# Performance work log

Hardware: AMD Instinct MI355X
Metric: run time of the kernel (lower is better)

Reference implementation:

```python
import jax, jax.numpy as jnp
import numpy as np

H = 8      # hidden_size
IN = 14    # input_size
B = 4096   # batch
T = 512    # seq_len
BN_EPS = 1e-5


def setup_inputs() -> dict:
    key = jax.random.key(0)
    ks = jax.random.split(key, 16)
    s = lambda k, shape, scale=0.25: jax.random.normal(k, shape, jnp.float32) * scale
    return {
        "x": jax.random.normal(ks[0], (B, T, IN), jnp.float32),
        # layer 1 LSTM params (PyTorch gate order: i, f, g, o)
        "Wih1": s(ks[1], (4 * H, IN)), "Whh1": s(ks[2], (4 * H, H)),
        "bih1": s(ks[3], (4 * H,)), "bhh1": s(ks[4], (4 * H,)),
        # layer 2 LSTM params
        "Wih2": s(ks[5], (4 * H, H)), "Whh2": s(ks[6], (4 * H, H)),
        "bih2": s(ks[7], (4 * H,)), "bhh2": s(ks[8], (4 * H,)),
        # BatchNorm1d(H) params + running stats (eval mode)
        "bn_gamma": jnp.ones((H,), jnp.float32), "bn_beta": jnp.zeros((H,), jnp.float32),
        "bn_mean": s(ks[9], (H,), 0.01), "bn_var": jnp.ones((H,), jnp.float32),
        # MLP head
        "w1": s(ks[10], (4, H)), "b1": s(ks[11], (4,)),
        "w2": s(ks[12], (1, 4)), "b2": s(ks[13], (1,)),
    }


def _cell(gates, c):
    # gates: [B, 4H] pre-activation, PyTorch order i, f, g, o
    i, f, g, o = jnp.split(gates, 4, axis=-1)
    c_new = jax.nn.sigmoid(f) * c + jax.nn.sigmoid(i) * jnp.tanh(g)
    h_new = jax.nn.sigmoid(o) * jnp.tanh(c_new)
    return h_new, c_new


def _lstm_last(x, Wih1, Whh1, bih1, bhh1, Wih2, Whh2, bih2, bhh2):
    # x: [B, T, IN] -> returns last hidden state of layer 2: [B, H]
    xt = jnp.swapaxes(x, 0, 1)  # [T, B, IN]
    # precompute input projections for layer 1 in one big GEMM
    xp1 = jnp.einsum('tbf,gf->tbg', xt, Wih1) + (bih1 + bhh1)  # [T, B, 4H]
    b2sum = bih2 + bhh2
    Bn = x.shape[0]
    z = jnp.zeros((Bn, H), x.dtype)
    init = (z, z, z, z)  # h1, c1, h2, c2

    def step(carry, xp):
        h1, c1, h2, c2 = carry
        h1, c1 = _cell(xp + h1 @ Whh1.T, c1)
        h2, c2 = _cell(h1 @ Wih2.T + h2 @ Whh2.T + b2sum, c2)
        return (h1, c1, h2, c2), None

    (h1, c1, h2, c2), _ = jax.lax.scan(step, init, xp1)
    return h2


def reference(x, Wih1, Whh1, bih1, bhh1, Wih2, Whh2, bih2, bhh2,
              bn_gamma, bn_beta, bn_mean, bn_var, w1, b1, w2, b2):
    last = _lstm_last(x, Wih1, Whh1, bih1, bhh1, Wih2, Whh2, bih2, bhh2)  # [B, H]
    # BatchNorm1d in eval mode (running stats); dropout is identity in eval
    normed = bn_gamma * (last - bn_mean) / jnp.sqrt(bn_var + BN_EPS) + bn_beta
    h = jax.nn.relu(normed @ w1.T + b1)  # [B, 4]
    out = h @ w2.T + b2                  # [B, 1]
    return out.squeeze(-1)               # [B]
```

## Files before the change

### kernel.cpp

```cpp
#include <hip/hip_runtime.h>

#define T_SEQ 512
#define INPUT 14
#define HID 8
#define GATES 32
#define TC 16
#define NCHUNK (T_SEQ / TC)
#define BN_EPS 1e-5f

__device__ __forceinline__ float fast_exp2(float x) { return __builtin_amdgcn_exp2f(x); }
__device__ __forceinline__ float fast_rcp(float x)  { return __builtin_amdgcn_rcpf(x); }

__global__ __launch_bounds__(256, 2)
void lstm_forex_kernel(const float* __restrict__ x,
                       const float* __restrict__ Wih1, const float* __restrict__ Whh1,
                       const float* __restrict__ bih1, const float* __restrict__ bhh1,
                       const float* __restrict__ Wih2, const float* __restrict__ Whh2,
                       const float* __restrict__ bih2, const float* __restrict__ bhh2,
                       const float* __restrict__ bn_gamma, const float* __restrict__ bn_beta,
                       const float* __restrict__ bn_mean, const float* __restrict__ bn_var,
                       const float* __restrict__ w1p, const float* __restrict__ b1p,
                       const float* __restrict__ w2p, const float* __restrict__ b2p,
                       float* __restrict__ out)
{
    __shared__ float xbuf[4][2][TC][16];
    __shared__ float gbuf[4][2][GATES];
    __shared__ float hbuf1[4][2][8];
    __shared__ float hbuf2[4][2][8];

    const int tid  = threadIdx.x;
    const int wave = tid >> 6;
    const int lane = tid & 63;
    const int grp  = lane >> 5;
    const int g    = lane & 31;
    const int unit = g & 7;
    const int type = g >> 3;

    const int b = blockIdx.x * 8 + wave * 2 + grp;

    float wi1[INPUT], wh1[HID], wi2[HID], wh2[HID];
#pragma unroll
    for (int k = 0; k < INPUT; ++k) wi1[k] = Wih1[g * INPUT + k];
#pragma unroll
    for (int j = 0; j < HID; ++j) wh1[j] = Whh1[g * HID + j];
#pragma unroll
    for (int j = 0; j < HID; ++j) wi2[j] = Wih2[g * HID + j];
#pragma unroll
    for (int j = 0; j < HID; ++j) wh2[j] = Whh2[g * HID + j];
    const float bsum1 = bih1[g] + bhh1[g];
    const float bsum2 = bih2[g] + bhh2[g];

    const float actScale = (type == 2) ? -2.885390082f : -1.4426950408f;
    const float actMul   = (type == 2) ? 2.f : 1.f;
    const float actAdd   = (type == 2) ? -1.f : 0.f;

    const float* gptr[7];
    int loff[7];
#pragma unroll
    for (int it = 0; it < 7; ++it) {
        int d   = it * 64 + lane;
        int es  = d / 224;
        int idx = d - es * 224;
        int tr  = idx / 14;
        int k   = idx - tr * 14;
        int bb  = blockIdx.x * 8 + wave * 2 + es;
        gptr[it] = x + (size_t)bb * (T_SEQ * INPUT) + idx;
        loff[it] = es * (TC * 16) + tr * 16 + k;
    }

    float h1[HID], h2v[HID];
    float c1 = 0.f, c2 = 0.f;
#pragma unroll
    for (int j = 0; j < HID; ++j) { h1[j] = 0.f; h2v[j] = 0.f; }

    float st[7];
#pragma unroll
    for (int it = 0; it < 7; ++it) { st[it] = *gptr[it]; gptr[it] += TC * INPUT; }

    float (*xw)[TC][16] = xbuf[wave];
    float* gw  = gbuf[wave][grp];
    float* h1w = hbuf1[wave][grp];
    float* h2w = hbuf2[wave][grp];

    for (int c = 0; c < NCHUNK; ++c) {
#pragma unroll
        for (int it = 0; it < 7; ++it) ((float*)xw)[loff[it]] = st[it];
        if (c + 1 < NCHUNK) {
#pragma unroll
            for (int it = 0; it < 7; ++it) { st[it] = *gptr[it]; gptr[it] += TC * INPUT; }
        }
        __builtin_amdgcn_wave_barrier();

#pragma unroll
        for (int t = 0; t < TC; ++t) {
            const float* xrow = &xw[grp][t][0];
            float4 xa = *(const float4*)(xrow + 0);
            float4 xb = *(const float4*)(xrow + 4);
            float4 xc = *(const float4*)(xrow + 8);
            float2 xd = *(const float2*)(xrow + 12);

            float a0 = bsum1, a1 = 0.f;
            a0 = fmaf(xa.x, wi1[0], a0);  a1 = fmaf(xa.y, wi1[1], a1);
            a0 = fmaf(xa.z, wi1[2], a0);  a1 = fmaf(xa.w, wi1[3], a1);
            a0 = fmaf(xb.x, wi1[4], a0);  a1 = fmaf(xb.y, wi1[5], a1);
            a0 = fmaf(xb.z, wi1[6], a0);  a1 = fmaf(xb.w, wi1[7], a1);
            a0 = fmaf(xc.x, wi1[8], a0);  a1 = fmaf(xc.y, wi1[9], a1);
            a0 = fmaf(xc.z, wi1[10], a0); a1 = fmaf(xc.w, wi1[11], a1);
            a0 = fmaf(xd.x, wi1[12], a0); a1 = fmaf(xd.y, wi1[13], a1);
#pragma unroll
            for (int j = 0; j < HID; j += 2) {
                a0 = fmaf(h1[j],     wh1[j],     a0);
                a1 = fmaf(h1[j + 1], wh1[j + 1], a1);
            }
            float acc = a0 + a1;

            float av = fmaf(fast_rcp(1.f + fast_exp2(actScale * acc)), actMul, actAdd);
            gw[(unit << 2) + type] = av;
            __builtin_amdgcn_wave_barrier();
            float4 gv = *(const float4*)&gw[unit << 2];
            c1 = fmaf(gv.y, c1, gv.x * gv.z);
            float th1 = fmaf(fast_rcp(1.f + fast_exp2(-2.885390082f * c1)), 2.f, -1.f);
            float hn1 = gv.w * th1;
            if (type == 0) h1w[unit] = hn1;
            __builtin_amdgcn_wave_barrier();
            float4 ha = *(const float4*)&h1w[0];
            float4 hb = *(const float4*)&h1w[4];
            h1[0] = ha.x; h1[1] = ha.y; h1[2] = ha.z; h1[3] = ha.w;
            h1[4] = hb.x; h1[5] = hb.y; h1[6] = hb.z; h1[7] = hb.w;

            float p0 = bsum2, p1 = 0.f;
#pragma unroll
            for (int j = 0; j < HID; j += 2) {
                p0 = fmaf(h1[j],      wi2[j],     p0);
                p1 = fmaf(h1[j + 1],  wi2[j + 1], p1);
            }
#pragma unroll
            for (int j = 0; j < HID; j += 2) {
                p0 = fmaf(h2v[j],     wh2[j],     p0);
                p1 = fmaf(h2v[j + 1], wh2[j + 1], p1);
            }
            float acc2 = p0 + p1;

            float av2 = fmaf(fast_rcp(1.f + fast_exp2(actScale * acc2)), actMul, actAdd);
            __builtin_amdgcn_wave_barrier();
            gw[(unit << 2) + type] = av2;
            __builtin_amdgcn_wave_barrier();
            float4 gv2 = *(const float4*)&gw[unit << 2];
            c2 = fmaf(gv2.y, c2, gv2.x * gv2.z);
            float th2 = fmaf(fast_rcp(1.f + fast_exp2(-2.885390082f * c2)), 2.f, -1.f);
            float hn2 = gv2.w * th2;
            if (type == 0) h2w[unit] = hn2;
            __builtin_amdgcn_wave_barrier();
            float4 h2a = *(const float4*)&h2w[0];
            float4 h2b = *(const float4*)&h2w[4];
            h2v[0] = h2a.x; h2v[1] = h2a.y; h2v[2] = h2a.z; h2v[3] = h2a.w;
            h2v[4] = h2b.x; h2v[5] = h2b.y; h2v[6] = h2b.z; h2v[7] = h2b.w;
        }
    }

    if (g == 0) {
        float nd[HID];
#pragma unroll
        for (int j = 0; j < HID; ++j) {
            float inv = 1.f / sqrtf(bn_var[j] + BN_EPS);
            nd[j] = bn_gamma[j] * (h2v[j] - bn_mean[j]) * inv + bn_beta[j];
        }
        float acc = b2p[0];
#pragma unroll
        for (int m = 0; m < 4; ++m) {
            float s = b1p[m];
#pragma unroll
            for (int j = 0; j < HID; ++j) s = fmaf(nd[j], w1p[m * HID + j], s);
            s = fmaxf(s, 0.f);
            acc = fmaf(s, w2p[m], acc);
        }
        out[b] = acc;
    }
}

extern "C" void kernel_launch(void* const* d_in, const int* in_sizes, int n_in,
                              void* d_out, int out_size, void* d_ws, size_t ws_size,
                              hipStream_t stream) {
    const float* x        = (const float*)d_in[0];
    const float* Wih1     = (const float*)d_in[1];
    const float* Whh1     = (const float*)d_in[2];
    const float* bih1     = (const float*)d_in[3];
    const float* bhh1     = (const float*)d_in[4];
    const float* Wih2     = (const float*)d_in[5];
    const float* Whh2     = (const float*)d_in[6];
    const float* bih2     = (const float*)d_in[7];
    const float* bhh2     = (const float*)d_in[8];
    const float* bn_gamma = (const float*)d_in[9];
    const float* bn_beta  = (const float*)d_in[10];
    const float* bn_mean  = (const float*)d_in[11];
    const float* bn_var   = (const float*)d_in[12];
    const float* w1p      = (const float*)d_in[13];
    const float* b1p      = (const float*)d_in[14];
    const float* w2p      = (const float*)d_in[15];
    const float* b2p      = (const float*)d_in[16];
    float* out = (float*)d_out;

    const int B = in_sizes[0] / (T_SEQ * INPUT);
    dim3 grid(B / 8), block(256);
    hipLaunchKernelGGL(lstm_forex_kernel, grid, block, 0, stream,
                       x, Wih1, Whh1, bih1, bhh1, Wih2, Whh2, bih2, bhh2,
                       bn_gamma, bn_beta, bn_mean, bn_var, w1p, b1p, w2p, b2p, out);
}
```

Measured before the change: 365.6 us.

## Exchange LSTM gates and hidden state via ds_swizzle instead of LDS

Replaces the shared-memory gate and hidden-state exchange buffers, along with their wave barriers, with ds_swizzle lane shuffles. Each lane computes its cell-state contribution from swizzled gate values, and the hidden vectors are broadcast to all lanes by swizzle. The layer-2 recurrent dot product with h2 is moved ahead of the layer-1 activation so it can overlap with the layer-1 critical path. This adds redundant cell computation on every lane and depends on the exact swizzle masks being correct.

```diff
diff --git a/kernel.cpp b/kernel.cpp
--- a/kernel.cpp
+++ b/kernel.cpp
@@ -3,13 +3,17 @@
 #define T_SEQ 512
 #define INPUT 14
 #define HID 8
-#define GATES 32
 #define TC 16
 #define NCHUNK (T_SEQ / TC)
 #define BN_EPS 1e-5f
 
 __device__ __forceinline__ float fast_exp2(float x) { return __builtin_amdgcn_exp2f(x); }
 __device__ __forceinline__ float fast_rcp(float x)  { return __builtin_amdgcn_rcpf(x); }
+
+template <int IMM>
+__device__ __forceinline__ float swz(float v) {
+    return __int_as_float(__builtin_amdgcn_ds_swizzle(__float_as_int(v), IMM));
+}
 
 __global__ __launch_bounds__(256, 2)
 void lstm_forex_kernel(const float* __restrict__ x,
@@ -24,17 +28,15 @@
                        float* __restrict__ out)
 {
     __shared__ float xbuf[4][2][TC][16];
-    __shared__ float gbuf[4][2][GATES];
-    __shared__ float hbuf1[4][2][8];
-    __shared__ float hbuf2[4][2][8];
 
     const int tid  = threadIdx.x;
     const int wave = tid >> 6;
     const int lane = tid & 63;
     const int grp  = lane >> 5;
     const int g    = lane & 31;
-    const int unit = g & 7;
     const int type = g >> 3;
+    const bool b0  = (type & 1) != 0;
+    const bool b1  = (type & 2) != 0;
 
     const int b = blockIdx.x * 8 + wave * 2 + grp;
 
@@ -78,9 +80,6 @@
     for (int it = 0; it < 7; ++it) { st[it] = *gptr[it]; gptr[it] += TC * INPUT; }
 
     float (*xw)[TC][16] = xbuf[wave];
-    float* gw  = gbuf[wave][grp];
-    float* h1w = hbuf1[wave][grp];
-    float* h2w = hbuf2[wave][grp];
 
     for (int c = 0; c < NCHUNK; ++c) {
 #pragma unroll
@@ -107,6 +106,12 @@
             a0 = fmaf(xc.x, wi1[8], a0);  a1 = fmaf(xc.y, wi1[9], a1);
             a0 = fmaf(xc.z, wi1[10], a0); a1 = fmaf(xc.w, wi1[11], a1);
             a0 = fmaf(xd.x, wi1[12], a0); a1 = fmaf(xd.y, wi1[13], a1);
+            float q0 = bsum2, q1 = 0.f;
+#pragma unroll
+            for (int j = 0; j < HID; j += 2) {
+                q0 = fmaf(h2v[j],     wh2[j],     q0);
+                q1 = fmaf(h2v[j + 1], wh2[j + 1], q1);
+            }
 #pragma unroll
             for (int j = 0; j < HID; j += 2) {
                 a0 = fmaf(h1[j],     wh1[j],     a0);
@@ -114,47 +119,43 @@
             }
             float acc = a0 + a1;
 
-            float av = fmaf(fast_rcp(1.f + fast_exp2(actScale * acc)), actMul, actAdd);
-            gw[(unit << 2) + type] = av;
-            __builtin_amdgcn_wave_barrier();
-            float4 gv = *(const float4*)&gw[unit << 2];
-            c1 = fmaf(gv.y, c1, gv.x * gv.z);
+            float v0 = fmaf(fast_rcp(1.f + fast_exp2(actScale * acc)), actMul, actAdd);
+            float v1 = swz<0x201F>(v0);
+            float v2 = swz<0x401F>(v0);
+            float v3 = swz<0x601F>(v0);
+            float P = b0 ? v1 * v3 : v0 * v2;
+            float F = b1 ? (b0 ? v2 : v3) : (b0 ? v0 : v1);
+            float O = b1 ? (b0 ? v0 : v1) : (b0 ? v2 : v3);
+            c1 = fmaf(F, c1, P);
             float th1 = fmaf(fast_rcp(1.f + fast_exp2(-2.885390082f * c1)), 2.f, -1.f);
-            float hn1 = gv.w * th1;
-            if (type == 0) h1w[unit] = hn1;
-            __builtin_amdgcn_wave_barrier();
-            float4 ha = *(const float4*)&h1w[0];
-            float4 hb = *(const float4*)&h1w[4];
-            h1[0] = ha.x; h1[1] = ha.y; h1[2] = ha.z; h1[3] = ha.w;
-            h1[4] = hb.x; h1[5] = hb.y; h1[6] = hb.z; h1[7] = hb.w;
-
-            float p0 = bsum2, p1 = 0.f;
+            float h1u = O * th1;
+            h1[0] = swz<0x18>(h1u); h1[1] = swz<0x38>(h1u);
+            h1[2] = swz<0x58>(h1u); h1[3] = swz<0x78>(h1u);
+            h1[4] = swz<0x98>(h1u); h1[5] = swz<0xB8>(h1u);
+            h1[6] = swz<0xD8>(h1u); h1[7] = swz<0xF8>(h1u);
+
+            float p0 = q0, p1 = q1;
 #pragma unroll
             for (int j = 0; j < HID; j += 2) {
-                p0 = fmaf(h1[j],      wi2[j],     p0);
-                p1 = fmaf(h1[j + 1],  wi2[j + 1], p1);
-            }
-#pragma unroll
-            for (int j = 0; j < HID; j += 2) {
-                p0 = fmaf(h2v[j],     wh2[j],     p0);
-                p1 = fmaf(h2v[j + 1], wh2[j + 1], p1);
+                p0 = fmaf(h1[j],     wi2[j],     p0);
+                p1 = fmaf(h1[j + 1], wi2[j + 1], p1);
             }
             float acc2 = p0 + p1;
 
-            float av2 = fmaf(fast_rcp(1.f + fast_exp2(actScale * acc2)), actMul, actAdd);
-            __builtin_amdgcn_wave_barrier();
-            gw[(unit << 2) + type] = av2;
-            __builtin_amdgcn_wave_barrier();
-            float4 gv2 = *(const float4*)&gw[unit << 2];
-            c2 = fmaf(gv2.y, c2, gv2.x * gv2.z);
+            float u0 = fmaf(fast_rcp(1.f + fast_exp2(actScale * acc2)), actMul, actAdd);
+            float u1 = swz<0x201F>(u0);
+            float u2 = swz<0x401F>(u0);
+            float u3 = swz<0x601F>(u0);
+            float P2 = b0 ? u1 * u3 : u0 * u2;
+            float F2 = b1 ? (b0 ? u2 : u3) : (b0 ? u0 : u1);
+            float O2 = b1 ? (b0 ? u0 : u1) : (b0 ? u2 : u3);
+            c2 = fmaf(F2, c2, P2);
             float th2 = fmaf(fast_rcp(1.f + fast_exp2(-2.885390082f * c2)), 2.f, -1.f);
-            float hn2 = gv2.w * th2;
-            if (type == 0) h2w[unit] = hn2;
-            __builtin_amdgcn_wave_barrier();
-            float4 h2a = *(const float4*)&h2w[0];
-            float4 h2b = *(const float4*)&h2w[4];
-            h2v[0] = h2a.x; h2v[1] = h2a.y; h2v[2] = h2a.z; h2v[3] = h2a.w;
-            h2v[4] = h2b.x; h2v[5] = h2b.y; h2v[6] = h2b.z; h2v[7] = h2b.w;
+            float h2u = O2 * th2;
+            h2v[0] = swz<0x18>(h2u); h2v[1] = swz<0x38>(h2u);
+            h2v[2] = swz<0x58>(h2u); h2v[3] = swz<0x78>(h2u);
+            h2v[4] = swz<0x98>(h2u); h2v[5] = swz<0xB8>(h2u);
+            h2v[6] = swz<0xD8>(h2u); h2v[7] = swz<0xF8>(h2u);
         }
     }
 
```

Result: faster. 353.0 us (-3.4%).
